# Kernel tuning notes

Measured on AMD Instinct MI355X. Metric: run time of the kernel, lower is better.

The kernel has to match this reference:

```python
import jax, jax.numpy as jnp
import numpy as np

N, E, F_IN, HID, HEADS, OUT, G = 50000, 800000, 128, 64, 4, 10, 64
NEG_SLOPE = 0.2


def _glorot(key, shape):
    fan = shape[0] + shape[-1]
    lim = np.sqrt(6.0 / fan)
    return jax.random.uniform(key, shape, jnp.float32, -lim, lim)


def setup_inputs() -> dict:
    key = jax.random.key(0)
    ks = jax.random.split(key, 20)
    x = jax.random.normal(ks[0], (N, F_IN), jnp.float32)
    edge_index = jax.random.randint(ks[1], (2, E), 0, N, jnp.int64)
    batch = jnp.sort(jax.random.randint(ks[2], (N,), 0, G, jnp.int64))
    inp = {"x": x, "edge_index": edge_index, "batch": batch}
    # layer 1: in=F_IN, heads=HEADS, out=HID
    inp["W1"] = _glorot(ks[3], (F_IN, HEADS * HID))
    inp["b1"] = jnp.zeros((HEADS * HID,), jnp.float32)
    inp["as1"] = _glorot(ks[4], (HEADS, HID))
    inp["ad1"] = _glorot(ks[5], (HEADS, HID))
    # layer 2: in=HEADS*HID, heads=HEADS, out=HID
    inp["W2"] = _glorot(ks[6], (HEADS * HID, HEADS * HID))
    inp["b2"] = jnp.zeros((HEADS * HID,), jnp.float32)
    inp["as2"] = _glorot(ks[7], (HEADS, HID))
    inp["ad2"] = _glorot(ks[8], (HEADS, HID))
    # layer 3: in=HEADS*HID, heads=1, out=HID
    inp["W3"] = _glorot(ks[9], (HEADS * HID, HID))
    inp["b3"] = jnp.zeros((HID,), jnp.float32)
    inp["as3"] = _glorot(ks[10], (1, HID))
    inp["ad3"] = _glorot(ks[11], (1, HID))
    # MLP head [HID, HID, OUT]
    inp["Wm1"] = _glorot(ks[12], (HID, HID))
    inp["bm1"] = jnp.zeros((HID,), jnp.float32)
    inp["Wm2"] = _glorot(ks[13], (HID, OUT))
    inp["bm2"] = jnp.zeros((OUT,), jnp.float32)
    return inp


def _gat_layer(x, src, dst, W, b, att_src, att_dst):
    # x: [N, Fin]; att_*: [H, C]
    H, C = att_src.shape
    h = (x @ W).reshape(N, H, C)
    a_src = jnp.einsum("nhc,hc->nh", h, att_src)
    a_dst = jnp.einsum("nhc,hc->nh", h, att_dst)
    alpha = jax.nn.leaky_relu(a_src[src] + a_dst[dst], NEG_SLOPE)  # [E', H]
    amax = jax.ops.segment_max(alpha, dst, num_segments=N)
    alpha = jnp.exp(alpha - amax[dst])
    denom = jax.ops.segment_sum(alpha, dst, num_segments=N)
    alpha = alpha / (denom[dst] + 1e-16)
    msg = h[src] * alpha[:, :, None]  # [E', H, C]
    out = jax.ops.segment_sum(msg, dst, num_segments=N)  # [N, H, C]
    return out.reshape(N, H * C) + b


def reference(x, edge_index, batch, W1, b1, as1, ad1, W2, b2, as2, ad2, W3, b3, as3, ad3, Wm1, bm1, Wm2, bm2):
    # PyG GATConv adds self-loops by default
    loops = jnp.arange(N, dtype=edge_index.dtype)
    src = jnp.concatenate([edge_index[0], loops])
    dst = jnp.concatenate([edge_index[1], loops])
    h = jax.nn.relu(_gat_layer(x, src, dst, W1, b1, as1, ad1))
    h = jax.nn.relu(_gat_layer(h, src, dst, W2, b2, as2, ad2))
    h = jax.nn.relu(_gat_layer(h, src, dst, W3, b3, as3, ad3))
    pooled = jax.ops.segment_sum(h, batch, num_segments=G)  # [G, HID]
    hidden = jax.nn.relu(pooled @ Wm1 + bm1)
    return hidden @ Wm2 + bm2
```

## Files before the change

### kernel.cpp

```cpp
#include <hip/hip_runtime.h>
#include <hip/hip_bf16.h>

#define F_IN   128
#define HID    64
#define HEADS  4
#define OUTD   10
#define NGRP   64

typedef unsigned short u16;
typedef __attribute__((ext_vector_type(8))) short short8;
typedef __attribute__((ext_vector_type(4))) float f32x4;

__device__ __forceinline__ float atomAddF(float* p, float v) {
    return __hip_atomic_fetch_add(p, v, __ATOMIC_RELAXED, __HIP_MEMORY_SCOPE_AGENT);
}
__device__ __forceinline__ float lrelu(float f) { return f > 0.f ? f : 0.2f * f; }
__device__ __forceinline__ float b2f(u16 u) { return __uint_as_float(((unsigned)u) << 16); }
__device__ __forceinline__ u16 f2b(float f) {
    unsigned u = __float_as_uint(f);
    return (u16)((u + 0x7fffu + ((u >> 16) & 1u)) >> 16);
}
__device__ __forceinline__ unsigned fmono(float f) {
    unsigned u = __float_as_uint(f);
    return (u & 0x80000000u) ? ~u : (u | 0x80000000u);
}
__device__ __forceinline__ float funmono(unsigned u) {
    return __uint_as_float((u & 0x80000000u) ? (u & 0x7FFFFFFFu) : ~u);
}

__global__ __launch_bounds__(256) void wtrans_all_kernel(const float* __restrict__ W1,
                                                         const float* __restrict__ W2,
                                                         const float* __restrict__ W3,
                                                         u16* __restrict__ Wt1,
                                                         u16* __restrict__ Wt2,
                                                         u16* __restrict__ Wt3) {
    int i = blockIdx.x * 256 + threadIdx.x;
    if (i < 32768) {
        int n = i >> 7, k = i & 127;
        Wt1[i] = f2b(W1[(size_t)k * 256 + n]);
    } else if (i < 98304) {
        int j = i - 32768;
        int n = j >> 8, k = j & 255;
        Wt2[j] = f2b(W2[(size_t)k * 256 + n]);
    } else if (i < 114688) {
        int j = i - 98304;
        int n = j >> 8, k = j & 255;
        Wt3[j] = f2b(W3[(size_t)k * 64 + n]);
    }
}

template<int K, int NC, bool AF32>
__global__ __launch_bounds__(512) void gemm_att_kernel(const void* __restrict__ Aptr,
                                                       const u16* __restrict__ Bt,
                                                       const float* __restrict__ as_,
                                                       const float* __restrict__ ad_,
                                                       u16* __restrict__ Hb,
                                                       float* __restrict__ a_src,
                                                       float* __restrict__ a_dst,
                                                       int nrows) {
    constexpr int LDA = 40;
    constexpr int HH = NC / 64;
    __shared__ u16 As[128][LDA];
    __shared__ u16 Bs[NC][LDA];
    int tid = threadIdx.x;
    int m0 = blockIdx.x * 128;
    int w = tid >> 6, l = tid & 63, lr = l & 15, lk = l >> 4;

    if constexpr (NC == 256) {
        int wr = w >> 2, wc = w & 3;
        f32x4 acc[4][4] = {};
        for (int k0 = 0; k0 < K; k0 += 32) {
            {
                int row = tid >> 2, ks = (tid & 3) * 8;
                int grow = m0 + row;
                short8 av = {};
                if (grow < nrows) {
                    if constexpr (AF32) {
                        const float* src = (const float*)Aptr + (size_t)grow * K + k0 + ks;
                        float4 v0 = *(const float4*)src;
                        float4 v1 = *(const float4*)(src + 4);
                        av[0] = (short)f2b(v0.x); av[1] = (short)f2b(v0.y);
                        av[2] = (short)f2b(v0.z); av[3] = (short)f2b(v0.w);
                        av[4] = (short)f2b(v1.x); av[5] = (short)f2b(v1.y);
                        av[6] = (short)f2b(v1.z); av[7] = (short)f2b(v1.w);
                    } else {
                        av = *(const short8*)&((const u16*)Aptr)[(size_t)grow * K + k0 + ks];
                    }
                }
                *(short8*)&As[row][ks] = av;
            }
            #pragma unroll
            for (int i = 0; i < 2; i++) {
                int col = (tid >> 2) + 128 * i;
                int ks = (tid & 3) * 8;
                *(short8*)&Bs[col][ks] = *(const short8*)&Bt[(size_t)col * K + k0 + ks];
            }
            __syncthreads();
            short8 a[4], b[4];
            #pragma unroll
            for (int mi = 0; mi < 4; mi++) a[mi] = *(const short8*)&As[64 * wr + 16 * mi + lr][lk * 8];
            #pragma unroll
            for (int ni = 0; ni < 4; ni++) b[ni] = *(const short8*)&Bs[64 * wc + 16 * ni + lr][lk * 8];
            #pragma unroll
            for (int mi = 0; mi < 4; mi++)
                #pragma unroll
                for (int ni = 0; ni < 4; ni++)
                    acc[mi][ni] = __builtin_amdgcn_mfma_f32_16x16x32_bf16(a[mi], b[ni], acc[mi][ni], 0, 0, 0);
            __syncthreads();
        }
        #pragma unroll
        for (int mi = 0; mi < 4; mi++) {
            #pragma unroll
            for (int j = 0; j < 4; j++) {
                int grow = m0 + 64 * wr + 16 * mi + lk * 4 + j;
                if (grow < nrows) {
                    #pragma unroll
                    for (int ni = 0; ni < 4; ni++)
                        Hb[(size_t)grow * NC + 64 * wc + 16 * ni + lr] = f2b(acc[mi][ni][j]);
                }
            }
        }
        float asv[4], adv[4];
        #pragma unroll
        for (int ni = 0; ni < 4; ni++) {
            asv[ni] = as_[wc * 64 + 16 * ni + lr];
            adv[ni] = ad_[wc * 64 + 16 * ni + lr];
        }
        #pragma unroll
        for (int mi = 0; mi < 4; mi++) {
            #pragma unroll
            for (int j = 0; j < 4; j++) {
                float ps = 0.f, pd = 0.f;
                #pragma unroll
                for (int ni = 0; ni < 4; ni++) {
                    float v = acc[mi][ni][j];
                    ps += v * asv[ni];
                    pd += v * adv[ni];
                }
                #pragma unroll
                for (int o = 1; o < 16; o <<= 1) {
                    ps += __shfl_xor(ps, o, 64);
                    pd += __shfl_xor(pd, o, 64);
                }
                int grow = m0 + 64 * wr + 16 * mi + lk * 4 + j;
                if (lr == 0 && grow < nrows) {
                    a_src[grow * HH + wc] = ps;
                    a_dst[grow * HH + wc] = pd;
                }
            }
        }
    } else {
        f32x4 acc[4] = {};
        for (int k0 = 0; k0 < K; k0 += 32) {
            {
                int row = tid >> 2, ks = (tid & 3) * 8;
                int grow = m0 + row;
                short8 av = {};
                if (grow < nrows) av = *(const short8*)&((const u16*)Aptr)[(size_t)grow * K + k0 + ks];
                *(short8*)&As[row][ks] = av;
            }
            if (tid < 256) {
                int col = tid >> 2;
                int ks = (tid & 3) * 8;
                *(short8*)&Bs[col][ks] = *(const short8*)&Bt[(size_t)col * K + k0 + ks];
            }
            __syncthreads();
            short8 af = *(const short8*)&As[16 * w + lr][lk * 8];
            #pragma unroll
            for (int c = 0; c < 4; c++) {
                short8 bf = *(const short8*)&Bs[c * 16 + lr][lk * 8];
                acc[c] = __builtin_amdgcn_mfma_f32_16x16x32_bf16(af, bf, acc[c], 0, 0, 0);
            }
            __syncthreads();
        }
        #pragma unroll
        for (int c = 0; c < 4; c++) {
            #pragma unroll
            for (int j = 0; j < 4; j++) {
                int grow = m0 + 16 * w + lk * 4 + j;
                if (grow < nrows) Hb[(size_t)grow * NC + c * 16 + lr] = f2b(acc[c][j]);
            }
        }
        float asv[4], adv[4];
        #pragma unroll
        for (int c = 0; c < 4; c++) {
            asv[c] = as_[c * 16 + lr];
            adv[c] = ad_[c * 16 + lr];
        }
        #pragma unroll
        for (int j = 0; j < 4; j++) {
            float ps = 0.f, pd = 0.f;
            #pragma unroll
            for (int c = 0; c < 4; c++) {
                float v = acc[c][j];
                ps += v * asv[c];
                pd += v * adv[c];
            }
            #pragma unroll
            for (int o = 1; o < 16; o <<= 1) {
                ps += __shfl_xor(ps, o, 64);
                pd += __shfl_xor(pd, o, 64);
            }
            int grow = m0 + 16 * w + lk * 4 + j;
            if (lr == 0 && grow < nrows) {
                a_src[grow] = ps;
                a_dst[grow] = pd;
            }
        }
    }
}

template<int HH>
__global__ __launch_bounds__(256) void gmax_kernel(const float* __restrict__ a_src,
                                                   unsigned* __restrict__ gmaxu, int n_nodes) {
    float mx[HH];
    #pragma unroll
    for (int h = 0; h < HH; h++) mx[h] = -3.4e38f;
    for (int i = blockIdx.x * 256 + threadIdx.x; i < n_nodes; i += gridDim.x * 256) {
        #pragma unroll
        for (int h = 0; h < HH; h++) mx[h] = fmaxf(mx[h], a_src[i * HH + h]);
    }
    #pragma unroll
    for (int h = 0; h < HH; h++) {
        #pragma unroll
        for (int off = 32; off; off >>= 1) mx[h] = fmaxf(mx[h], __shfl_xor(mx[h], off, 64));
    }
    if ((threadIdx.x & 63) == 0) {
        #pragma unroll
        for (int h = 0; h < HH; h++) atomicMax(&gmaxu[h], fmono(mx[h]));
    }
}

__global__ void count_kernel(const int* __restrict__ ei, int* __restrict__ deg,
                             int E_, int n_nodes) {
    int e = blockIdx.x * 256 + threadIdx.x;
    int tot = E_ + n_nodes;
    if (e >= tot) return;
    int d = (e < E_) ? ei[E_ + e] : e - E_;
    atomicAdd(&deg[d], 1);
}

__global__ __launch_bounds__(256) void scan_reduce_kernel(const int* __restrict__ deg,
                                                          int* __restrict__ bsum, int n) {
    int i = blockIdx.x * 256 + threadIdx.x;
    int v = (i < n) ? deg[i] : 0;
    #pragma unroll
    for (int o = 32; o; o >>= 1) v += __shfl_xor(v, o, 64);
    __shared__ int ws[4];
    if ((threadIdx.x & 63) == 0) ws[threadIdx.x >> 6] = v;
    __syncthreads();
    if (threadIdx.x == 0) bsum[blockIdx.x] = ws[0] + ws[1] + ws[2] + ws[3];
}

__global__ __launch_bounds__(256) void scan_blocksums_kernel(int* __restrict__ bsum, int nb) {
    __shared__ int s[256];
    int t = threadIdx.x;
    int v = (t < nb) ? bsum[t] : 0;
    s[t] = v;
    __syncthreads();
    #pragma unroll
    for (int d = 1; d < 256; d <<= 1) {
        int x = (t >= d) ? s[t - d] : 0;
        __syncthreads();
        s[t] += x;
        __syncthreads();
    }
    if (t < nb) bsum[t] = s[t] - v;
}

__global__ __launch_bounds__(256) void scan_final_kernel(const int* __restrict__ deg,
                                                         const int* __restrict__ bsum,
                                                         int* __restrict__ off, int n) {
    __shared__ int s[256];
    int t = threadIdx.x;
    int i = blockIdx.x * 256 + t;
    int v = (i < n) ? deg[i] : 0;
    s[t] = v;
    __syncthreads();
    #pragma unroll
    for (int d = 1; d < 256; d <<= 1) {
        int x = (t >= d) ? s[t - d] : 0;
        __syncthreads();
        s[t] += x;
        __syncthreads();
    }
    int ex = s[t] - v + bsum[blockIdx.x];
    if (i < n) off[i] = ex;
    if (i == n - 1) off[n] = ex + v;
}

__global__ void fill_part_kernel(const int* __restrict__ ei, const int* __restrict__ off,
                                 int* __restrict__ cursor, int* __restrict__ csr_src,
                                 int E_, int n_nodes, int d_lo, int d_hi) {
    int e = blockIdx.x * 256 + threadIdx.x;
    int tot = E_ + n_nodes;
    if (e >= tot) return;
    int s, d;
    if (e < E_) { s = ei[e]; d = ei[E_ + e]; } else { s = d = e - E_; }
    if (d < d_lo || d >= d_hi) return;
    int pos = atomicAdd(&cursor[d], 1);
    csr_src[off[d] + pos] = s;
}

__global__ __launch_bounds__(256) void gat_aggr_kernel(const int* __restrict__ off,
                                                       const int* __restrict__ csr_src,
                                                       const u16* __restrict__ Hb,
                                                       const float* __restrict__ a_src,
                                                       const float* __restrict__ a_dst,
                                                       const unsigned* __restrict__ gmaxu,
                                                       const float* __restrict__ bias,
                                                       u16* __restrict__ outb16,
                                                       int n_nodes) {
    constexpr int HH = 4, HC = 256;
    int d = blockIdx.x * 4 + (threadIdx.x >> 6);
    if (d >= n_nodes) return;
    int lane = threadIdx.x & 63;
    int hh = lane >> 4;
    int g = lane & 15;
    int gb = lane & 48;
    int o0 = off[d];
    int deg = off[d + 1] - o0;
    float adm = a_dst[d * HH + hh];
    float m = lrelu(funmono(gmaxu[hh]) + adm);

    float den = 0.f;
    float acc[4] = {};
    int j = 0;
    for (; j + 4 <= deg; j += 4) {
        int s0 = csr_src[o0 + j + 0];
        int s1 = csr_src[o0 + j + 1];
        int s2 = csr_src[o0 + j + 2];
        int s3 = csr_src[o0 + j + 3];
        int ssel = s3;
        if (g == 0) ssel = s0; else if (g == 1) ssel = s1; else if (g == 2) ssel = s2;
        float e = __expf(lrelu(a_src[ssel * HH + hh] + adm) - m);
        float e0 = __shfl(e, gb + 0, 64);
        float e1 = __shfl(e, gb + 1, 64);
        float e2 = __shfl(e, gb + 2, 64);
        float e3 = __shfl(e, gb + 3, 64);
        den += (e0 + e1) + (e2 + e3);
        uint2 h0 = *(const uint2*)&Hb[(size_t)s0 * HC + lane * 4];
        uint2 h1 = *(const uint2*)&Hb[(size_t)s1 * HC + lane * 4];
        uint2 h2 = *(const uint2*)&Hb[(size_t)s2 * HC + lane * 4];
        uint2 h3 = *(const uint2*)&Hb[(size_t)s3 * HC + lane * 4];
        acc[0] += e0 * __uint_as_float(h0.x << 16) + e1 * __uint_as_float(h1.x << 16)
                + e2 * __uint_as_float(h2.x << 16) + e3 * __uint_as_float(h3.x << 16);
        acc[1] += e0 * __uint_as_float(h0.x & 0xffff0000u) + e1 * __uint_as_float(h1.x & 0xffff0000u)
                + e2 * __uint_as_float(h2.x & 0xffff0000u) + e3 * __uint_as_float(h3.x & 0xffff0000u);
        acc[2] += e0 * __uint_as_float(h0.y << 16) + e1 * __uint_as_float(h1.y << 16)
                + e2 * __uint_as_float(h2.y << 16) + e3 * __uint_as_float(h3.y << 16);
        acc[3] += e0 * __uint_as_float(h0.y & 0xffff0000u) + e1 * __uint_as_float(h1.y & 0xffff0000u)
                + e2 * __uint_as_float(h2.y & 0xffff0000u) + e3 * __uint_as_float(h3.y & 0xffff0000u);
    }
    for (; j < deg; j++) {
        int s = csr_src[o0 + j];
        float al = __expf(lrelu(a_src[s * HH + hh] + adm) - m);
        den += al;
        uint2 hv = *(const uint2*)&Hb[(size_t)s * HC + lane * 4];
        acc[0] += al * __uint_as_float(hv.x << 16);
        acc[1] += al * __uint_as_float(hv.x & 0xffff0000u);
        acc[2] += al * __uint_as_float(hv.y << 16);
        acc[3] += al * __uint_as_float(hv.y & 0xffff0000u);
    }
    float inv = 1.f / (den + 1e-16f);
    float4 bv = *(const float4*)&bias[lane * 4];
    float v0 = fmaxf(acc[0] * inv + bv.x, 0.f);
    float v1 = fmaxf(acc[1] * inv + bv.y, 0.f);
    float v2 = fmaxf(acc[2] * inv + bv.z, 0.f);
    float v3 = fmaxf(acc[3] * inv + bv.w, 0.f);
    uint2 o;
    o.x = (unsigned)f2b(v0) | ((unsigned)f2b(v1) << 16);
    o.y = (unsigned)f2b(v2) | ((unsigned)f2b(v3) << 16);
    *(uint2*)&outb16[(size_t)d * HC + lane * 4] = o;
}

__global__ __launch_bounds__(256) void gat_aggr3_kernel(const int* __restrict__ off,
                                                        const int* __restrict__ csr_src,
                                                        const u16* __restrict__ Hb,
                                                        const float* __restrict__ a_src,
                                                        const float* __restrict__ a_dst,
                                                        const unsigned* __restrict__ gmaxu,
                                                        const float* __restrict__ bias,
                                                        float* __restrict__ outf32,
                                                        int n_nodes) {
    int d = blockIdx.x * 4 + (threadIdx.x >> 6);
    if (d >= n_nodes) return;
    int lane = threadIdx.x & 63;
    int grp = lane >> 4;
    int li = lane & 15;
    int o0 = off[d];
    int deg = off[d + 1] - o0;
    float adm = a_dst[d];
    float m = lrelu(funmono(gmaxu[0]) + adm);

    float den = 0.f;
    float a0 = 0.f, a1 = 0.f, a2 = 0.f, a3 = 0.f;
    int j = 0;
    for (; j + 8 <= deg; j += 8) {
        int sA = csr_src[o0 + j + grp];
        int sB = csr_src[o0 + j + 4 + grp];
        float alA = __expf(lrelu(a_src[sA] + adm) - m);
        float alB = __expf(lrelu(a_src[sB] + adm) - m);
        uint2 hA = *(const uint2*)&Hb[(size_t)sA * 64 + li * 4];
        uint2 hB = *(const uint2*)&Hb[(size_t)sB * 64 + li * 4];
        den += alA + alB;
        a0 += alA * __uint_as_float(hA.x << 16) + alB * __uint_as_float(hB.x << 16);
        a1 += alA * __uint_as_float(hA.x & 0xffff0000u) + alB * __uint_as_float(hB.x & 0xffff0000u);
        a2 += alA * __uint_as_float(hA.y << 16) + alB * __uint_as_float(hB.y << 16);
        a3 += alA * __uint_as_float(hA.y & 0xffff0000u) + alB * __uint_as_float(hB.y & 0xffff0000u);
    }
    for (; j < deg; j += 4) {
        int e = j + grp;
        float al = 0.f;
        unsigned hx = 0u, hy = 0u;
        if (e < deg) {
            int s = csr_src[o0 + e];
            al = __expf(lrelu(a_src[s] + adm) - m);
            uint2 hv = *(const uint2*)&Hb[(size_t)s * 64 + li * 4];
            hx = hv.x; hy = hv.y;
        }
        den += al;
        a0 += al * __uint_as_float(hx << 16);
        a1 += al * __uint_as_float(hx & 0xffff0000u);
        a2 += al * __uint_as_float(hy << 16);
        a3 += al * __uint_as_float(hy & 0xffff0000u);
    }
    #pragma unroll
    for (int o = 16; o < 64; o <<= 1) {
        den += __shfl_xor(den, o, 64);
        a0  += __shfl_xor(a0, o, 64);
        a1  += __shfl_xor(a1, o, 64);
        a2  += __shfl_xor(a2, o, 64);
        a3  += __shfl_xor(a3, o, 64);
    }
    if (grp == 0) {
        float inv = 1.f / (den + 1e-16f);
        float4 bv = *(const float4*)&bias[li * 4];
        float4 o;
        o.x = fmaxf(a0 * inv + bv.x, 0.f);
        o.y = fmaxf(a1 * inv + bv.y, 0.f);
        o.z = fmaxf(a2 * inv + bv.z, 0.f);
        o.w = fmaxf(a3 * inv + bv.w, 0.f);
        *(float4*)&outf32[(size_t)d * 64 + li * 4] = o;
    }
}

__global__ __launch_bounds__(256) void pool_kernel(const float* __restrict__ H3,
                                                   const int* __restrict__ batch,
                                                   float* __restrict__ pooled, int n_nodes) {
    int wave = (blockIdx.x * 256 + threadIdx.x) >> 6;
    int lane = threadIdx.x & 63;
    int nwaves = gridDim.x * 4;
    int chunk = (n_nodes + nwaves - 1) / nwaves;
    int start = wave * chunk;
    int end = min(n_nodes, start + chunk);
    if (start >= end) return;
    int cur = batch[start];
    float acc = 0.f;
    for (int n = start; n < end; n++) {
        int g = batch[n];
        if (g != cur) { atomAddF(&pooled[cur * 64 + lane], acc); acc = 0.f; cur = g; }
        acc += H3[(size_t)n * 64 + lane];
    }
    atomAddF(&pooled[cur * 64 + lane], acc);
}

__global__ __launch_bounds__(64) void mlp_kernel(const float* __restrict__ pooled,
                                                 const float* __restrict__ Wm1,
                                                 const float* __restrict__ bm1,
                                                 const float* __restrict__ Wm2,
                                                 const float* __restrict__ bm2,
                                                 float* __restrict__ out) {
    __shared__ float sp[64], sh[64];
    int g = blockIdx.x, t = threadIdx.x;
    sp[t] = pooled[g * 64 + t];
    __syncthreads();
    float a = bm1[t];
    for (int k = 0; k < 64; k++) a += sp[k] * Wm1[k * 64 + t];
    sh[t] = a > 0.f ? a : 0.f;
    __syncthreads();
    if (t < 10) {
        float o = bm2[t];
        for (int j = 0; j < 64; j++) o += sh[j] * Wm2[j * 10 + t];
        out[g * 10 + t] = o;
    }
}

extern "C" void kernel_launch(void* const* d_in, const int* in_sizes, int n_in,
                              void* d_out, int out_size, void* d_ws, size_t ws_size,
                              hipStream_t stream) {
    const float* x   = (const float*)d_in[0];
    const int*   ei  = (const int*)d_in[1];
    const int*   bat = (const int*)d_in[2];
    const float* W1  = (const float*)d_in[3];
    const float* b1  = (const float*)d_in[4];
    const float* as1 = (const float*)d_in[5];
    const float* ad1 = (const float*)d_in[6];
    const float* W2  = (const float*)d_in[7];
    const float* b2  = (const float*)d_in[8];
    const float* as2 = (const float*)d_in[9];
    const float* ad2 = (const float*)d_in[10];
    const float* W3  = (const float*)d_in[11];
    const float* b3  = (const float*)d_in[12];
    const float* as3 = (const float*)d_in[13];
    const float* ad3 = (const float*)d_in[14];
    const float* Wm1 = (const float*)d_in[15];
    const float* bm1 = (const float*)d_in[16];
    const float* Wm2 = (const float*)d_in[17];
    const float* bm2 = (const float*)d_in[18];
    float* out = (float*)d_out;

    const int Nn = in_sizes[0] / F_IN;
    const int Ee = in_sizes[1] / 2;
    const int Et = Ee + Nn;

    char* wsp = (char*)d_ws;
    size_t off_b = 0;
    auto alloc = [&](size_t bytes) { void* p = wsp + off_b; off_b += (bytes + 255) & ~(size_t)255; return p; };
    u16*   HbA     = (u16*)alloc((size_t)Nn * 256 * 2);
    u16*   HbB     = (u16*)alloc((size_t)Nn * 256 * 2);
    float* Hf      = (float*)alloc((size_t)Nn * HID * 4);
    u16*   Wt1     = (u16*)alloc((size_t)256 * 128 * 2);
    u16*   Wt2     = (u16*)alloc((size_t)256 * 256 * 2);
    u16*   Wt3     = (u16*)alloc((size_t)64 * 256 * 2);
    float* a_src   = (float*)alloc((size_t)Nn * HEADS * 4);
    float* a_dst   = (float*)alloc((size_t)Nn * HEADS * 4);
    size_t zcount = 16 + (size_t)Nn * 2 + NGRP * HID;
    unsigned* zbase = (unsigned*)alloc(zcount * 4);
    unsigned* gmaxu = zbase;
    int*   deg     = (int*)(zbase + 16);
    int*   cursor  = deg + Nn;
    float* pooled  = (float*)(cursor + Nn);
    int*   bsum    = (int*)alloc((size_t)256 * 4);
    int*   csr_off = (int*)alloc((size_t)(Nn + 1) * 4);
    int*   csr_src = (int*)alloc((size_t)Et * 4);
    (void)ws_size;

    wtrans_all_kernel<<<(114688 + 255) / 256, 256, 0, stream>>>(W1, W2, W3, Wt1, Wt2, Wt3);

    hipMemsetAsync(zbase, 0, zcount * 4, stream);

    int eb = (Et + 255) / 256;
    int nb = (Nn + 255) / 256;
    count_kernel<<<eb, 256, 0, stream>>>(ei, deg, Ee, Nn);
    scan_reduce_kernel<<<nb, 256, 0, stream>>>(deg, bsum, Nn);
    scan_blocksums_kernel<<<1, 256, 0, stream>>>(bsum, nb);
    scan_final_kernel<<<nb, 256, 0, stream>>>(deg, bsum, csr_off, Nn);
    {
        int q = (Nn + 3) / 4;
        for (int p = 0; p < 4; p++) {
            int lo = p * q, hi = min(Nn, lo + q);
            fill_part_kernel<<<eb, 256, 0, stream>>>(ei, csr_off, cursor, csr_src,
                                                     Ee, Nn, lo, hi);
        }
    }

    const int gemm_blocks = (Nn + 127) / 128;
    const int nodeBlocks = (Nn + 3) / 4;

    gemm_att_kernel<128, 256, true><<<gemm_blocks, 512, 0, stream>>>(x, Wt1, as1, ad1,
                                                                     HbA, a_src, a_dst, Nn);
    gmax_kernel<4><<<64, 256, 0, stream>>>(a_src, gmaxu + 0, Nn);
    gat_aggr_kernel<<<nodeBlocks, 256, 0, stream>>>(csr_off, csr_src, HbA,
                                                    a_src, a_dst, gmaxu + 0, b1, HbB, Nn);
    gemm_att_kernel<256, 256, false><<<gemm_blocks, 512, 0, stream>>>(HbB, Wt2, as2, ad2,
                                                                      HbA, a_src, a_dst, Nn);
    gmax_kernel<4><<<64, 256, 0, stream>>>(a_src, gmaxu + 4, Nn);
    gat_aggr_kernel<<<nodeBlocks, 256, 0, stream>>>(csr_off, csr_src, HbA,
                                                    a_src, a_dst, gmaxu + 4, b2, HbB, Nn);
    gemm_att_kernel<256, 64, false><<<gemm_blocks, 512, 0, stream>>>(HbB, Wt3, as3, ad3,
                                                                     HbA, a_src, a_dst, Nn);
    gmax_kernel<1><<<64, 256, 0, stream>>>(a_src, gmaxu + 8, Nn);
    gat_aggr3_kernel<<<nodeBlocks, 256, 0, stream>>>(csr_off, csr_src, HbA,
                                                     a_src, a_dst, gmaxu + 8, b3, Hf, Nn);

    pool_kernel<<<128, 256, 0, stream>>>(Hf, bat, pooled, Nn);
    mlp_kernel<<<NGRP, 64, 0, stream>>>(pooled, Wm1, bm1, Wm2, bm2, out);
}
```

Baseline: 395.9 us.

## Schedule aggregation nodes in descending-degree order via counting-sort permutation

Adds a histogram, scan and scatter pass that builds a permutation of destination nodes sorted by in-degree, highest first. The three aggregation kernels then process nodes through this permutation so each block's four wavefronts handle nodes of similar degree, and long nodes start early, which is meant to reduce load imbalance and tail effects. This adds three small kernels and an extra indirection, and it loses the sequential node order, which may hurt output write locality and off/a_dst access coalescing.

```diff
diff --git a/kernel.cpp b/kernel.cpp
--- a/kernel.cpp
+++ b/kernel.cpp
@@ -302,7 +302,24 @@
     csr_src[off[d] + pos] = s;
 }
 
-__global__ __launch_bounds__(256) void gat_aggr_kernel(const int* __restrict__ off,
+__global__ void hist_kernel(const int* __restrict__ deg, int* __restrict__ hist, int n) {
+    int i = blockIdx.x * 256 + threadIdx.x;
+    if (i >= n) return;
+    int b = 255 - min(deg[i], 255);
+    atomicAdd(&hist[b], 1);
+}
+
+__global__ void scatter_kernel(const int* __restrict__ deg, const int* __restrict__ hoff,
+                               int* __restrict__ hcur, int* __restrict__ perm, int n) {
+    int i = blockIdx.x * 256 + threadIdx.x;
+    if (i >= n) return;
+    int b = 255 - min(deg[i], 255);
+    int pos = atomicAdd(&hcur[b], 1);
+    perm[hoff[b] + pos] = i;
+}
+
+__global__ __launch_bounds__(256) void gat_aggr_kernel(const int* __restrict__ perm,
+                                                       const int* __restrict__ off,
                                                        const int* __restrict__ csr_src,
                                                        const u16* __restrict__ Hb,
                                                        const float* __restrict__ a_src,
@@ -312,8 +329,9 @@
                                                        u16* __restrict__ outb16,
                                                        int n_nodes) {
     constexpr int HH = 4, HC = 256;
-    int d = blockIdx.x * 4 + (threadIdx.x >> 6);
-    if (d >= n_nodes) return;
+    int idx = blockIdx.x * 4 + (threadIdx.x >> 6);
+    if (idx >= n_nodes) return;
+    int d = perm[idx];
     int lane = threadIdx.x & 63;
     int hh = lane >> 4;
     int g = lane & 15;
@@ -374,7 +392,8 @@
     *(uint2*)&outb16[(size_t)d * HC + lane * 4] = o;
 }
 
-__global__ __launch_bounds__(256) void gat_aggr3_kernel(const int* __restrict__ off,
+__global__ __launch_bounds__(256) void gat_aggr3_kernel(const int* __restrict__ perm,
+                                                        const int* __restrict__ off,
                                                         const int* __restrict__ csr_src,
                                                         const u16* __restrict__ Hb,
                                                         const float* __restrict__ a_src,
@@ -383,8 +402,9 @@
                                                         const float* __restrict__ bias,
                                                         float* __restrict__ outf32,
                                                         int n_nodes) {
-    int d = blockIdx.x * 4 + (threadIdx.x >> 6);
-    if (d >= n_nodes) return;
+    int idx = blockIdx.x * 4 + (threadIdx.x >> 6);
+    if (idx >= n_nodes) return;
+    int d = perm[idx];
     int lane = threadIdx.x & 63;
     int grp = lane >> 4;
     int li = lane & 15;
@@ -525,15 +545,18 @@
     u16*   Wt3     = (u16*)alloc((size_t)64 * 256 * 2);
     float* a_src   = (float*)alloc((size_t)Nn * HEADS * 4);
     float* a_dst   = (float*)alloc((size_t)Nn * HEADS * 4);
-    size_t zcount = 16 + (size_t)Nn * 2 + NGRP * HID;
+    size_t zcount = 16 + (size_t)Nn * 2 + NGRP * HID + 512;
     unsigned* zbase = (unsigned*)alloc(zcount * 4);
     unsigned* gmaxu = zbase;
     int*   deg     = (int*)(zbase + 16);
     int*   cursor  = deg + Nn;
     float* pooled  = (float*)(cursor + Nn);
+    int*   hist    = (int*)(pooled + NGRP * HID);
+    int*   hcur    = hist + 256;
     int*   bsum    = (int*)alloc((size_t)256 * 4);
     int*   csr_off = (int*)alloc((size_t)(Nn + 1) * 4);
     int*   csr_src = (int*)alloc((size_t)Et * 4);
+    int*   perm    = (int*)alloc((size_t)Nn * 4);
     (void)ws_size;
 
     wtrans_all_kernel<<<(114688 + 255) / 256, 256, 0, stream>>>(W1, W2, W3, Wt1, Wt2, Wt3);
@@ -554,6 +577,9 @@
                                                      Ee, Nn, lo, hi);
         }
     }
+    hist_kernel<<<nb, 256, 0, stream>>>(deg, hist, Nn);
+    scan_blocksums_kernel<<<1, 256, 0, stream>>>(hist, 256);
+    scatter_kernel<<<nb, 256, 0, stream>>>(deg, hist, hcur, perm, Nn);
 
     const int gemm_blocks = (Nn + 127) / 128;
     const int nodeBlocks = (Nn + 3) / 4;
@@ -561,17 +587,17 @@
     gemm_att_kernel<128, 256, true><<<gemm_blocks, 512, 0, stream>>>(x, Wt1, as1, ad1,
                                                                      HbA, a_src, a_dst, Nn);
     gmax_kernel<4><<<64, 256, 0, stream>>>(a_src, gmaxu + 0, Nn);
-    gat_aggr_kernel<<<nodeBlocks, 256, 0, stream>>>(csr_off, csr_src, HbA,
+    gat_aggr_kernel<<<nodeBlocks, 256, 0, stream>>>(perm, csr_off, csr_src, HbA,
                                                     a_src, a_dst, gmaxu + 0, b1, HbB, Nn);
     gemm_att_kernel<256, 256, false><<<gemm_blocks, 512, 0, stream>>>(HbB, Wt2, as2, ad2,
                                                                       HbA, a_src, a_dst, Nn);
     gmax_kernel<4><<<64, 256, 0, stream>>>(a_src, gmaxu + 4, Nn);
-    gat_aggr_kernel<<<nodeBlocks, 256, 0, stream>>>(csr_off, csr_src, HbA,
+    gat_aggr_kernel<<<nodeBlocks, 256, 0, stream>>>(perm, csr_off, csr_src, HbA,
                                                     a_src, a_dst, gmaxu + 4, b2, HbB, Nn);
     gemm_att_kernel<256, 64, false><<<gemm_blocks, 512, 0, stream>>>(HbB, Wt3, as3, ad3,
                                                                      HbA, a_src, a_dst, Nn);
     gmax_kernel<1><<<64, 256, 0, stream>>>(a_src, gmaxu + 8, Nn);
-    gat_aggr3_kernel<<<nodeBlocks, 256, 0, stream>>>(csr_off, csr_src, HbA,
+    gat_aggr3_kernel<<<nodeBlocks, 256, 0, stream>>>(perm, csr_off, csr_src, HbA,
                                                      a_src, a_dst, gmaxu + 8, b3, Hf, Nn);
 
     pool_kernel<<<128, 256, 0, stream>>>(Hf, bat, pooled, Nn);
```

After: 644.0 us. 62.7% more time.
